# Kernel tuning notes

Hardware: AMD Instinct MI355X
Metric: run time of the kernel (lower is better)

Reference implementation:

```python
import jax, jax.numpy as jnp
import numpy as np


def setup_inputs() -> dict:
    key = jax.random.key(0)
    k1, k2 = jax.random.split(key)
    p1 = jax.random.normal(k1, (4, 8192, 3), dtype=jnp.float32)
    p2 = jax.random.normal(k2, (4, 8192, 3), dtype=jnp.float32)
    return {"p1": p1, "p2": p2}


def reference(p1, p2):
    # dist[b, n, m] = ||p1[b, n] - p2[b, m]||^2  (faithful to broadcasted diff)
    diff = p1[:, :, None, :] - p2[:, None, :, :]          # [B, N, M, 3]
    dist = jnp.sum(diff * diff, axis=-1)                  # [B, N, M]
    p1_to_p2 = jnp.min(dist, axis=-1)                     # [B, N]
    p2_to_p1 = jnp.min(dist, axis=-2)                     # [B, M]
    chamfer = (p1_to_p2.mean(axis=-1) + p2_to_p1.mean(axis=-1)).mean()
    return chamfer
```

## Files before the change

### kernel.cpp

```cpp
#include <hip/hip_runtime.h>

#define THREADS 256
#define QPT 4
#define SLICES 8
#define NPTS 8192
#define BATCH 4
#define SLICE (NPTS / SLICES)


__global__ void chamfer_init(unsigned int* mins, float* out) {
    int i = blockIdx.x * blockDim.x + threadIdx.x;
    mins[i] = 0x7F800000u;
    if (i == 0) out[0] = 0.0f;
}

__global__ __launch_bounds__(THREADS) void chamfer_main(
    const float* __restrict__ p1, const float* __restrict__ p2,
    unsigned int* __restrict__ mins)
{
    const int tid  = threadIdx.x;
    const int bz   = blockIdx.z;
    const int dir  = bz >> 2;
    const int b    = bz & 3;
    const int qbase = blockIdx.x * (THREADS * QPT);
    const int tbase = blockIdx.y * SLICE;

    const float* __restrict__ qsrc = (dir == 0) ? p1 : p2;
    const float* __restrict__ tsrc = (dir == 0) ? p2 : p1;

    __shared__ float4 tgt[SLICE];
    {
        const float* tp = tsrc + ((size_t)b * NPTS + tbase) * 3;
        for (int k = tid; k < SLICE; k += THREADS) {
            float x = tp[k * 3 + 0];
            float y = tp[k * 3 + 1];
            float z = tp[k * 3 + 2];
            tgt[k] = make_float4(-2.0f * x, -2.0f * y, -2.0f * z,
                                 fmaf(x, x, fmaf(y, y, z * z)));
        }
    }

    float ax[QPT], ay[QPT], az[QPT], a2[QPT], best[QPT];
#pragma unroll
    for (int j = 0; j < QPT; ++j) {
        const int q = qbase + j * THREADS + tid;
        const float* qp = qsrc + ((size_t)b * NPTS + q) * 3;
        ax[j] = qp[0]; ay[j] = qp[1]; az[j] = qp[2];
        a2[j] = fmaf(ax[j], ax[j], fmaf(ay[j], ay[j], az[j] * az[j]));
        best[j] = 3.0e38f;
    }

    __syncthreads();

#pragma unroll 4
    for (int m = 0; m < SLICE; ++m) {
        float4 t = tgt[m];
#pragma unroll
        for (int j = 0; j < QPT; ++j) {
            float d = fmaf(ax[j], t.x, fmaf(ay[j], t.y, fmaf(az[j], t.z, t.w)));
            best[j] = fminf(best[j], d);
        }
    }

    unsigned int* mbase = mins + ((size_t)dir * BATCH + b) * NPTS;
#pragma unroll
    for (int j = 0; j < QPT; ++j) {
        float v = fmaxf(best[j] + a2[j], 0.0f);
        atomicMin(&mbase[qbase + j * THREADS + tid], __float_as_uint(v));
    }
}

__global__ __launch_bounds__(THREADS) void chamfer_reduce(
    const uint4* __restrict__ mins, float* __restrict__ out)
{
    const int i = blockIdx.x * THREADS + threadIdx.x;
    uint4 u = mins[i];
    float s = __uint_as_float(u.x) + __uint_as_float(u.y)
            + __uint_as_float(u.z) + __uint_as_float(u.w);
#pragma unroll
    for (int off = 32; off >= 1; off >>= 1)
        s += __shfl_down(s, off, 64);
    __shared__ float partial[THREADS / 64];
    if ((threadIdx.x & 63) == 0) partial[threadIdx.x >> 6] = s;
    __syncthreads();
    if (threadIdx.x == 0) {
        float tot = 0.0f;
#pragma unroll
        for (int w = 0; w < THREADS / 64; ++w) tot += partial[w];
        atomicAdd(out, tot * (1.0f / (BATCH * NPTS)));
    }
}

extern "C" void kernel_launch(void* const* d_in, const int* in_sizes, int n_in,
                              void* d_out, int out_size, void* d_ws, size_t ws_size,
                              hipStream_t stream) {
    const float* p1 = (const float*)d_in[0];
    const float* p2 = (const float*)d_in[1];
    unsigned int* mins = (unsigned int*)d_ws;
    float* out = (float*)d_out;

    chamfer_init<<<(2 * BATCH * NPTS) / THREADS, THREADS, 0, stream>>>(mins, out);

    dim3 grid(NPTS / (THREADS * QPT), SLICES, 2 * BATCH);
    chamfer_main<<<grid, THREADS, 0, stream>>>(p1, p2, mins);

    chamfer_reduce<<<(2 * BATCH * NPTS) / (4 * THREADS), THREADS, 0, stream>>>(
        (const uint4*)mins, out);
}
```

Baseline: 103.7 us.

## Split targets into more slices, raise per-thread queries, write per-slice partial minima

Doubles queries per thread to 8 and splits targets into 32 slices, which reuses each shared-memory target load across more queries and keeps the grid at 4x32x8 blocks. Each slice writes its own minima to a partials buffer, and a separate reduction takes the min across slices. This replaces global atomicMin and the init kernel whenever the workspace is large enough. The inner loop also handles two targets per iteration. The cost is a larger workspace (8 MB) and more global reads in the reduce, and register pressure goes up with QPT=8.

```diff
diff --git a/kernel.cpp b/kernel.cpp
--- a/kernel.cpp
+++ b/kernel.cpp
@@ -1,27 +1,26 @@
 #include <hip/hip_runtime.h>
 
 #define THREADS 256
-#define QPT 4
-#define SLICES 8
+#define QPT 8
+#define SLICES 32
 #define NPTS 8192
 #define BATCH 4
 #define SLICE (NPTS / SLICES)
 
 
-__global__ void chamfer_init(unsigned int* mins, float* out) {
+__global__ void chamfer_init(unsigned int* mins) {
     int i = blockIdx.x * blockDim.x + threadIdx.x;
     mins[i] = 0x7F800000u;
-    if (i == 0) out[0] = 0.0f;
 }
 
 __global__ __launch_bounds__(THREADS) void chamfer_main(
     const float* __restrict__ p1, const float* __restrict__ p2,
-    unsigned int* __restrict__ mins)
+    float* __restrict__ ws, int use_partials)
 {
     const int tid  = threadIdx.x;
-    const int bz   = blockIdx.z;
-    const int dir  = bz >> 2;
-    const int b    = bz & 3;
+    const int dirb = blockIdx.z;
+    const int dir  = dirb >> 2;
+    const int b    = dirb & 3;
     const int qbase = blockIdx.x * (THREADS * QPT);
     const int tbase = blockIdx.y * SLICE;
 
@@ -52,25 +51,62 @@
 
     __syncthreads();
 
-#pragma unroll 4
-    for (int m = 0; m < SLICE; ++m) {
-        float4 t = tgt[m];
+#pragma unroll 2
+    for (int m = 0; m < SLICE; m += 2) {
+        float4 ta = tgt[m];
+        float4 tb = tgt[m + 1];
 #pragma unroll
         for (int j = 0; j < QPT; ++j) {
-            float d = fmaf(ax[j], t.x, fmaf(ay[j], t.y, fmaf(az[j], t.z, t.w)));
-            best[j] = fminf(best[j], d);
+            float da = fmaf(ax[j], ta.x, fmaf(ay[j], ta.y, fmaf(az[j], ta.z, ta.w)));
+            float db = fmaf(ax[j], tb.x, fmaf(ay[j], tb.y, fmaf(az[j], tb.z, tb.w)));
+            best[j] = fminf(fminf(best[j], da), db);
         }
     }
 
-    unsigned int* mbase = mins + ((size_t)dir * BATCH + b) * NPTS;
+    if (use_partials) {
+        float* pbase = ws + (((size_t)blockIdx.y * 8 + dirb) * NPTS);
 #pragma unroll
-    for (int j = 0; j < QPT; ++j) {
-        float v = fmaxf(best[j] + a2[j], 0.0f);
-        atomicMin(&mbase[qbase + j * THREADS + tid], __float_as_uint(v));
+        for (int j = 0; j < QPT; ++j) {
+            float v = fmaxf(best[j] + a2[j], 0.0f);
+            pbase[qbase + j * THREADS + tid] = v;
+        }
+    } else {
+        unsigned int* mbase = (unsigned int*)ws + ((size_t)dirb * NPTS);
+#pragma unroll
+        for (int j = 0; j < QPT; ++j) {
+            float v = fmaxf(best[j] + a2[j], 0.0f);
+            atomicMin(&mbase[qbase + j * THREADS + tid], __float_as_uint(v));
+        }
     }
 }
 
-__global__ __launch_bounds__(THREADS) void chamfer_reduce(
+__global__ __launch_bounds__(THREADS) void chamfer_reduce_partials(
+    const float* __restrict__ partials, float* __restrict__ out)
+{
+    const int i = blockIdx.x * THREADS + threadIdx.x;
+    const int dirb = i >> 13;
+    const int q = i & (NPTS - 1);
+    float v = 3.4e38f;
+#pragma unroll 8
+    for (int s = 0; s < SLICES; ++s)
+        v = fminf(v, partials[((size_t)s * 8 + dirb) * NPTS + q]);
+
+    float sv = v;
+#pragma unroll
+    for (int off = 32; off >= 1; off >>= 1)
+        sv += __shfl_down(sv, off, 64);
+    __shared__ float partial[THREADS / 64];
+    if ((threadIdx.x & 63) == 0) partial[threadIdx.x >> 6] = sv;
+    __syncthreads();
+    if (threadIdx.x == 0) {
+        float tot = 0.0f;
+#pragma unroll
+        for (int w = 0; w < THREADS / 64; ++w) tot += partial[w];
+        atomicAdd(out, tot * (1.0f / (BATCH * NPTS)));
+    }
+}
+
+__global__ __launch_bounds__(THREADS) void chamfer_reduce_atomic(
     const uint4* __restrict__ mins, float* __restrict__ out)
 {
     const int i = blockIdx.x * THREADS + threadIdx.x;
@@ -96,14 +132,26 @@
                               hipStream_t stream) {
     const float* p1 = (const float*)d_in[0];
     const float* p2 = (const float*)d_in[1];
-    unsigned int* mins = (unsigned int*)d_ws;
     float* out = (float*)d_out;
 
-    chamfer_init<<<(2 * BATCH * NPTS) / THREADS, THREADS, 0, stream>>>(mins, out);
+    const size_t need_partials = (size_t)SLICES * 8 * NPTS * 4;
+    const int use_partials = (ws_size >= need_partials) ? 1 : 0;
+
+    hipMemsetAsync(d_out, 0, sizeof(float), stream);
+
+    if (!use_partials) {
+        chamfer_init<<<(2 * BATCH * NPTS) / THREADS, THREADS, 0, stream>>>(
+            (unsigned int*)d_ws);
+    }
 
     dim3 grid(NPTS / (THREADS * QPT), SLICES, 2 * BATCH);
-    chamfer_main<<<grid, THREADS, 0, stream>>>(p1, p2, mins);
+    chamfer_main<<<grid, THREADS, 0, stream>>>(p1, p2, (float*)d_ws, use_partials);
 
-    chamfer_reduce<<<(2 * BATCH * NPTS) / (4 * THREADS), THREADS, 0, stream>>>(
-        (const uint4*)mins, out);
+    if (use_partials) {
+        chamfer_reduce_partials<<<(2 * BATCH * NPTS) / THREADS, THREADS, 0, stream>>>(
+            (const float*)d_ws, out);
+    } else {
+        chamfer_reduce_atomic<<<(2 * BATCH * NPTS) / (4 * THREADS), THREADS, 0, stream>>>(
+            (const uint4*)d_ws, out);
+    }
 }
```

After: 107.4 us. 1.04x slower.

## Compute pairwise distances with bf16 split-precision MFMA instead of scalar FMA

Applied to the files above, without the earlier changes.

Recasts the distance computation as a matrix product. Each point and its squared norm are split into bf16 high and low parts and packed into K=16 operand rows, so one 32x32x16 MFMA yields 32x32 distance tiles at roughly fp32 accuracy. Each wave owns 32 query points, scans all targets without slicing, reduces the minima with shuffles and adds the result atomically. This removes the global atomicMin buffer and the init and reduce kernels, and adds a prep kernel that writes packed tables. Accuracy depends on the hi/lo split, and the cross terms dropped from the split leave a small residual error.

```diff
diff --git a/kernel.cpp b/kernel.cpp
--- a/kernel.cpp
+++ b/kernel.cpp
@@ -1,92 +1,140 @@
 #include <hip/hip_runtime.h>
 
 #define THREADS 256
-#define QPT 4
-#define SLICES 8
 #define NPTS 8192
 #define BATCH 4
-#define SLICE (NPTS / SLICES)
+#define NTILES (NPTS / 32)
+#define NTASKS (2 * BATCH * (NPTS / 32))
+#define NBLOCKS (NTASKS / 4)
+
+typedef short bf16x8 __attribute__((ext_vector_type(8)));
+typedef float f32x16 __attribute__((ext_vector_type(16)));
+
+#define BF16_ONE ((unsigned short)0x3F80)
+
+__device__ __forceinline__ unsigned short bf16_rne(float x) {
+    unsigned int u = __float_as_uint(x);
+    unsigned int r = u + 0x7FFFu + ((u >> 16) & 1u);
+    return (unsigned short)(r >> 16);
+}
+__device__ __forceinline__ float bf16_to_f(unsigned short h) {
+    return __uint_as_float(((unsigned int)h) << 16);
+}
 
 
-__global__ void chamfer_init(unsigned int* mins, float* out) {
-    int i = blockIdx.x * blockDim.x + threadIdx.x;
-    mins[i] = 0x7F800000u;
-    if (i == 0) out[0] = 0.0f;
-}
-
-__global__ __launch_bounds__(THREADS) void chamfer_main(
+__global__ __launch_bounds__(THREADS) void chamfer_prep(
     const float* __restrict__ p1, const float* __restrict__ p2,
-    unsigned int* __restrict__ mins)
+    unsigned short* __restrict__ atab, unsigned short* __restrict__ btab)
 {
-    const int tid  = threadIdx.x;
-    const int bz   = blockIdx.z;
-    const int dir  = bz >> 2;
-    const int b    = bz & 3;
-    const int qbase = blockIdx.x * (THREADS * QPT);
-    const int tbase = blockIdx.y * SLICE;
-
+    const int i = blockIdx.x * THREADS + threadIdx.x;
+    const int dirb = i >> 13;
+    const int p = i & (NPTS - 1);
+    const int dir = dirb >> 2, b = dirb & 3;
     const float* __restrict__ qsrc = (dir == 0) ? p1 : p2;
     const float* __restrict__ tsrc = (dir == 0) ? p2 : p1;
 
-    __shared__ float4 tgt[SLICE];
     {
-        const float* tp = tsrc + ((size_t)b * NPTS + tbase) * 3;
-        for (int k = tid; k < SLICE; k += THREADS) {
-            float x = tp[k * 3 + 0];
-            float y = tp[k * 3 + 1];
-            float z = tp[k * 3 + 2];
-            tgt[k] = make_float4(-2.0f * x, -2.0f * y, -2.0f * z,
-                                 fmaf(x, x, fmaf(y, y, z * z)));
-        }
+        const float* qp = qsrc + ((size_t)b * NPTS + p) * 3;
+        float x = qp[0], y = qp[1], z = qp[2];
+        unsigned short xh = bf16_rne(x), yh = bf16_rne(y), zh = bf16_rne(z);
+        unsigned short xl = bf16_rne(x - bf16_to_f(xh));
+        unsigned short yl = bf16_rne(y - bf16_to_f(yh));
+        unsigned short zl = bf16_rne(z - bf16_to_f(zh));
+        float q2 = fmaf(x, x, fmaf(y, y, z * z));
+        unsigned short q2h = bf16_rne(q2);
+        unsigned short q2l = bf16_rne(q2 - bf16_to_f(q2h));
+        unsigned short k[16] = {xh, xh, xl, xl, yh, yh, yl, yl,
+                                zh, zh, zl, zl, q2h, q2l, BF16_ONE, BF16_ONE};
+        uint4* dst = (uint4*)(atab + (size_t)i * 16);
+        uint4 w0, w1;
+        w0.x = (unsigned)k[0] | ((unsigned)k[1] << 16);
+        w0.y = (unsigned)k[2] | ((unsigned)k[3] << 16);
+        w0.z = (unsigned)k[4] | ((unsigned)k[5] << 16);
+        w0.w = (unsigned)k[6] | ((unsigned)k[7] << 16);
+        w1.x = (unsigned)k[8] | ((unsigned)k[9] << 16);
+        w1.y = (unsigned)k[10] | ((unsigned)k[11] << 16);
+        w1.z = (unsigned)k[12] | ((unsigned)k[13] << 16);
+        w1.w = (unsigned)k[14] | ((unsigned)k[15] << 16);
+        dst[0] = w0; dst[1] = w1;
     }
-
-    float ax[QPT], ay[QPT], az[QPT], a2[QPT], best[QPT];
-#pragma unroll
-    for (int j = 0; j < QPT; ++j) {
-        const int q = qbase + j * THREADS + tid;
-        const float* qp = qsrc + ((size_t)b * NPTS + q) * 3;
-        ax[j] = qp[0]; ay[j] = qp[1]; az[j] = qp[2];
-        a2[j] = fmaf(ax[j], ax[j], fmaf(ay[j], ay[j], az[j] * az[j]));
-        best[j] = 3.0e38f;
-    }
-
-    __syncthreads();
-
-#pragma unroll 4
-    for (int m = 0; m < SLICE; ++m) {
-        float4 t = tgt[m];
-#pragma unroll
-        for (int j = 0; j < QPT; ++j) {
-            float d = fmaf(ax[j], t.x, fmaf(ay[j], t.y, fmaf(az[j], t.z, t.w)));
-            best[j] = fminf(best[j], d);
-        }
-    }
-
-    unsigned int* mbase = mins + ((size_t)dir * BATCH + b) * NPTS;
-#pragma unroll
-    for (int j = 0; j < QPT; ++j) {
-        float v = fmaxf(best[j] + a2[j], 0.0f);
-        atomicMin(&mbase[qbase + j * THREADS + tid], __float_as_uint(v));
+    {
+        const float* tp = tsrc + ((size_t)b * NPTS + p) * 3;
+        float x = tp[0], y = tp[1], z = tp[2];
+        float u = -2.0f * x, v = -2.0f * y, w = -2.0f * z;
+        unsigned short uh = bf16_rne(u), vh = bf16_rne(v), wh = bf16_rne(w);
+        unsigned short ul = bf16_rne(u - bf16_to_f(uh));
+        unsigned short vl = bf16_rne(v - bf16_to_f(vh));
+        unsigned short wl = bf16_rne(w - bf16_to_f(wh));
+        float t2 = fmaf(x, x, fmaf(y, y, z * z));
+        unsigned short t2h = bf16_rne(t2);
+        unsigned short t2l = bf16_rne(t2 - bf16_to_f(t2h));
+        unsigned short k[16] = {uh, ul, uh, ul, vh, vl, vh, vl,
+                                wh, wl, wh, wl, BF16_ONE, BF16_ONE, t2h, t2l};
+        uint4* dst = (uint4*)(btab + (size_t)i * 16);
+        uint4 w0, w1;
+        w0.x = (unsigned)k[0] | ((unsigned)k[1] << 16);
+        w0.y = (unsigned)k[2] | ((unsigned)k[3] << 16);
+        w0.z = (unsigned)k[4] | ((unsigned)k[5] << 16);
+        w0.w = (unsigned)k[6] | ((unsigned)k[7] << 16);
+        w1.x = (unsigned)k[8] | ((unsigned)k[9] << 16);
+        w1.y = (unsigned)k[10] | ((unsigned)k[11] << 16);
+        w1.z = (unsigned)k[12] | ((unsigned)k[13] << 16);
+        w1.w = (unsigned)k[14] | ((unsigned)k[15] << 16);
+        dst[0] = w0; dst[1] = w1;
     }
 }
 
-__global__ __launch_bounds__(THREADS) void chamfer_reduce(
-    const uint4* __restrict__ mins, float* __restrict__ out)
+__global__ __launch_bounds__(THREADS) void chamfer_mfma(
+    const unsigned short* __restrict__ atab,
+    const unsigned short* __restrict__ btab,
+    float* __restrict__ out)
 {
-    const int i = blockIdx.x * THREADS + threadIdx.x;
-    uint4 u = mins[i];
-    float s = __uint_as_float(u.x) + __uint_as_float(u.y)
-            + __uint_as_float(u.z) + __uint_as_float(u.w);
+    const int wid  = threadIdx.x >> 6;
+    const int lane = threadIdx.x & 63;
+    const int half = lane >> 5;
+    const int ln   = lane & 31;
+    const int task = blockIdx.x * 4 + wid;
+    const int dirb = task >> 8;
+    const int g    = task & 255;
+
+    const bf16x8* __restrict__ af = (const bf16x8*)atab;
+    const bf16x8* __restrict__ bfp = (const bf16x8*)btab
+        + (size_t)dirb * NPTS * 2 + (size_t)ln * 2 + half;
+
+    bf16x8 a = af[((size_t)dirb * NPTS + (size_t)g * 32 + ln) * 2 + half];
+
+    f32x16 zc = {0.f, 0.f, 0.f, 0.f, 0.f, 0.f, 0.f, 0.f,
+                 0.f, 0.f, 0.f, 0.f, 0.f, 0.f, 0.f, 0.f};
+    float best[16];
 #pragma unroll
-    for (int off = 32; off >= 1; off >>= 1)
-        s += __shfl_down(s, off, 64);
-    __shared__ float partial[THREADS / 64];
-    if ((threadIdx.x & 63) == 0) partial[threadIdx.x >> 6] = s;
+    for (int r = 0; r < 16; ++r) best[r] = 3.0e38f;
+
+#pragma unroll 2
+    for (int t = 0; t < NTILES; ++t) {
+        bf16x8 bfr = bfp[t * 64];
+        f32x16 acc = __builtin_amdgcn_mfma_f32_32x32x16_bf16(a, bfr, zc, 0, 0, 0);
+#pragma unroll
+        for (int r = 0; r < 16; ++r) best[r] = fminf(best[r], acc[r]);
+    }
+
+#pragma unroll
+    for (int m = 16; m >= 1; m >>= 1) {
+#pragma unroll
+        for (int r = 0; r < 16; ++r)
+            best[r] = fminf(best[r], __shfl_xor(best[r], m, 64));
+    }
+
+    float s = 0.0f;
+#pragma unroll
+    for (int r = 0; r < 16; ++r) s += fmaxf(best[r], 0.0f);
+
+    __shared__ float psum[8];
+    if (ln == 0) psum[wid * 2 + half] = s;
     __syncthreads();
     if (threadIdx.x == 0) {
         float tot = 0.0f;
 #pragma unroll
-        for (int w = 0; w < THREADS / 64; ++w) tot += partial[w];
+        for (int k = 0; k < 8; ++k) tot += psum[k];
         atomicAdd(out, tot * (1.0f / (BATCH * NPTS)));
     }
 }
@@ -96,14 +144,15 @@
                               hipStream_t stream) {
     const float* p1 = (const float*)d_in[0];
     const float* p2 = (const float*)d_in[1];
-    unsigned int* mins = (unsigned int*)d_ws;
     float* out = (float*)d_out;
 
-    chamfer_init<<<(2 * BATCH * NPTS) / THREADS, THREADS, 0, stream>>>(mins, out);
+    unsigned short* atab = (unsigned short*)d_ws;
+    unsigned short* btab = atab + (size_t)2 * BATCH * NPTS * 16;
 
-    dim3 grid(NPTS / (THREADS * QPT), SLICES, 2 * BATCH);
-    chamfer_main<<<grid, THREADS, 0, stream>>>(p1, p2, mins);
+    hipMemsetAsync(d_out, 0, sizeof(float), stream);
 
-    chamfer_reduce<<<(2 * BATCH * NPTS) / (4 * THREADS), THREADS, 0, stream>>>(
-        (const uint4*)mins, out);
+    chamfer_prep<<<(2 * BATCH * NPTS) / THREADS, THREADS, 0, stream>>>(
+        p1, p2, atab, btab);
+
+    chamfer_mfma<<<NBLOCKS, THREADS, 0, stream>>>(atab, btab, out);
 }
```

After: 114.6 us. +10.6%, slower.
